# Optimization experiments

Hardware: AMD Instinct MI355X
Metric: run time of the kernel (lower is better)

Reference implementation:

```python
import jax, jax.numpy as jnp
from jax import lax
import numpy as np

VOCAB, TAGS, EMB, HID = 50000, 45, 256, 512
B, S = 32, 256


def setup_inputs() -> dict:
    key = jax.random.key(0)
    ks = jax.random.split(key, 12)
    sc = 0.05
    return {
        "x": jax.random.randint(ks[0], (B, S), 0, VOCAB),
        "tags": jax.random.randint(ks[1], (B, S), 0, TAGS),
        "emb": jax.random.normal(ks[2], (VOCAB, EMB), jnp.float32) * sc,
        "w_ih_f": jax.random.normal(ks[3], (4 * HID, EMB), jnp.float32) * sc,
        "w_hh_f": jax.random.normal(ks[4], (4 * HID, HID), jnp.float32) * sc,
        "b_f": jnp.zeros((4 * HID,), jnp.float32),
        "w_ih_b": jax.random.normal(ks[5], (4 * HID, EMB), jnp.float32) * sc,
        "w_hh_b": jax.random.normal(ks[6], (4 * HID, HID), jnp.float32) * sc,
        "b_b": jnp.zeros((4 * HID,), jnp.float32),
        "lin_w": jax.random.normal(ks[7], (TAGS, 2 * HID), jnp.float32) * sc,
        "lin_b": jnp.zeros((TAGS,), jnp.float32),
        "start_t": jax.random.normal(ks[8], (TAGS,), jnp.float32) * 0.1,
        "end_t": jax.random.normal(ks[9], (TAGS,), jnp.float32) * 0.1,
        "trans": jax.random.normal(ks[10], (TAGS,), jnp.float32)[:, None] * 0.0 + jax.random.normal(ks[11], (TAGS, TAGS), jnp.float32) * 0.1,
    }


def _lstm_dir(xs, w_ih, w_hh, b, reverse):
    # xs: [B,S,E]. PyTorch gate order: i, f, g, o.
    Bsz = xs.shape[0]
    H = w_hh.shape[1]
    def step(carry, x_t):
        h, c = carry
        g = x_t @ w_ih.T + h @ w_hh.T + b
        i, f, gg, o = jnp.split(g, 4, axis=-1)
        c = jax.nn.sigmoid(f) * c + jax.nn.sigmoid(i) * jnp.tanh(gg)
        h = jax.nn.sigmoid(o) * jnp.tanh(c)
        return (h, c), h
    init = (jnp.zeros((Bsz, H), xs.dtype), jnp.zeros((Bsz, H), xs.dtype))
    _, hs = lax.scan(step, init, jnp.swapaxes(xs, 0, 1), reverse=reverse)
    return jnp.swapaxes(hs, 0, 1)  # [B,S,H]


def _crf_nll(em, tags, start_t, end_t, trans):
    # em: [B,S,T]; numerator: score of gold path
    em_sc = jnp.take_along_axis(em, tags[..., None], axis=2)[..., 0].sum(axis=1)
    tr_sc = trans[tags[:, :-1], tags[:, 1:]].sum(axis=1)
    score = start_t[tags[:, 0]] + em_sc + tr_sc + end_t[tags[:, -1]]
    # partition function via forward algorithm (logsumexp recurrence)
    alpha0 = start_t + em[:, 0]  # [B,T]
    def step(alpha, e_t):
        alpha = jax.nn.logsumexp(alpha[:, :, None] + trans[None], axis=1) + e_t
        return alpha, None
    alpha, _ = lax.scan(step, alpha0, jnp.swapaxes(em[:, 1:], 0, 1))
    logZ = jax.nn.logsumexp(alpha + end_t, axis=1)
    return -(score - logZ).mean()  # reduction='mean', loss = -llh


def reference(x, tags, emb, w_ih_f, w_hh_f, b_f, w_ih_b, w_hh_b, b_b,
              lin_w, lin_b, start_t, end_t, trans):
    embeds = emb[x]                               # [B,S,E]
    h_f = _lstm_dir(embeds, w_ih_f, w_hh_f, b_f, False)
    h_b = _lstm_dir(embeds, w_ih_b, w_hh_b, b_b, True)
    lstm_out = jnp.concatenate([h_f, h_b], axis=-1)  # [B,S,2H]
    emissions = lstm_out @ lin_w.T + lin_b           # [B,S,T]
    return _crf_nll(emissions, tags, start_t, end_t, trans)
```

## Files before the change

kernel.cpp:

```cpp
#include <hip/hip_runtime.h>

#define BB 32
#define SS 256
#define EMBD 256
#define HIDD 512
#define NTAG 45
#define TPAD 48
#define NBLK 32
#define APAD 520
#define GRID_REC 256

typedef __bf16 bf16x8 __attribute__((ext_vector_type(8)));
typedef float  f32x4  __attribute__((ext_vector_type(4)));
typedef short  s16x8  __attribute__((ext_vector_type(8)));
typedef short  s16x4  __attribute__((ext_vector_type(4)));

__device__ __forceinline__ unsigned short f2bf(float x) {
  unsigned u = __builtin_bit_cast(unsigned, x);
  u = (u + 0x7fffu + ((u >> 16) & 1u)) >> 16;
  return (unsigned short)u;
}
__device__ __forceinline__ float bf2f(unsigned short u) {
  unsigned v = ((unsigned)u) << 16; return __builtin_bit_cast(float, v);
}
__device__ __forceinline__ float ftanh(float x) {
  float e = __expf(2.f * x);
  return 1.f - 2.f / (e + 1.f);
}

__device__ __forceinline__ unsigned ld32_cpol(const unsigned* p, bool sys) {
  unsigned v;
  if (sys) asm volatile("global_load_dword %0, %1, off sc0 sc1\ns_waitcnt vmcnt(0)"
                        : "=v"(v) : "v"(p) : "memory");
  else     asm volatile("global_load_dword %0, %1, off sc0\ns_waitcnt vmcnt(0)"
                        : "=v"(v) : "v"(p) : "memory");
  return v;
}
__device__ __forceinline__ void st32_cpol(unsigned* p, unsigned v, bool sys) {
  if (sys) asm volatile("global_store_dword %0, %1, off sc0 sc1" :: "v"(p), "v"(v) : "memory");
  else     asm volatile("global_store_dword %0, %1, off sc0"     :: "v"(p), "v"(v) : "memory");
}

#define LD8(CPOL)                                                           \
  asm volatile("global_load_dwordx4 %0, %[q0], off " CPOL "\n\t"            \
               "global_load_dwordx4 %1, %[q1], off " CPOL "\n\t"            \
               "global_load_dwordx4 %2, %[q2], off " CPOL "\n\t"            \
               "global_load_dwordx4 %3, %[q3], off " CPOL "\n\t"            \
               "global_load_dwordx4 %4, %[q4], off " CPOL "\n\t"            \
               "global_load_dwordx4 %5, %[q5], off " CPOL "\n\t"            \
               "global_load_dwordx4 %6, %[q6], off " CPOL "\n\t"            \
               "global_load_dwordx4 %7, %[q7], off " CPOL "\n\t"            \
               "s_waitcnt vmcnt(0)"                                         \
               : "=&v"(v0), "=&v"(v1), "=&v"(v2), "=&v"(v3),                \
                 "=&v"(v4), "=&v"(v5), "=&v"(v6), "=&v"(v7)                 \
               : [q0] "v"(p), [q1] "v"(p + 2048), [q2] "v"(p + 4096),       \
                 [q3] "v"(p + 6144), [q4] "v"(p + 8192), [q5] "v"(p + 10240),\
                 [q6] "v"(p + 12288), [q7] "v"(p + 14336)                   \
               : "memory")

__global__ void k_pack_e(const int* __restrict__ x, const float* __restrict__ emb,
                         unsigned short* __restrict__ E) {
  int idx = blockIdx.x * 256 + threadIdx.x;
  int e = idx & 255; int bt = idx >> 8; int b = bt & 31; int t = bt >> 5;
  int tok = x[b * SS + t];
  E[idx] = f2bf(emb[(long)tok * EMBD + e]);
}

__global__ void k_pack_w(const float* __restrict__ wih_f, const float* __restrict__ whh_f,
                         const float* __restrict__ bf_,  const float* __restrict__ wih_b,
                         const float* __restrict__ whh_b, const float* __restrict__ bb_,
                         unsigned short* __restrict__ Wh, unsigned short* __restrict__ Wie,
                         float* __restrict__ Bh) {
  long idx = (long)blockIdx.x * 256 + threadIdx.x;
  int k = (int)(idx % 768); long rest = idx / 768;
  int r2 = (int)(rest & 2047); int dir = (int)(rest >> 11);
  int blk = r2 >> 6, rl = r2 & 63, gate = rl >> 4, hl = rl & 15;
  int orig = gate * HIDD + blk * 16 + hl;
  const float* wih = dir ? wih_b : wih_f;
  const float* whh = dir ? whh_b : whh_f;
  if (k < HIDD) Wh[((long)(dir * 2048 + r2)) * 512 + k] = f2bf(whh[(long)orig * HIDD + k]);
  else          Wie[((long)(dir * 2048 + r2)) * 256 + (k - 512)] = f2bf(wih[(long)orig * EMBD + (k - 512)]);
  if (k == 0) {
    const float* bias = dir ? bb_ : bf_;
    Bh[dir * 2048 + r2] = bias[orig];
  }
}

__global__ void k_pack_l(const float* __restrict__ lin_w, const float* __restrict__ lin_b,
                         unsigned short* __restrict__ LW, float* __restrict__ LB) {
  int idx = blockIdx.x * 256 + threadIdx.x;
  if (idx < TPAD * 1024) {
    int tag = idx >> 10; int c = idx & 1023;
    LW[idx] = (tag < NTAG) ? f2bf(lin_w[tag * 1024 + c]) : (unsigned short)0;
  } else if (idx < TPAD * 1024 + TPAD) {
    int tag = idx - TPAD * 1024;
    LB[tag] = (tag < NTAG) ? lin_b[tag] : 0.f;
  }
}

__launch_bounds__(256)
__global__ void k_eproj(const unsigned short* __restrict__ E,
                        const unsigned short* __restrict__ Wie,
                        const float* __restrict__ Bh,
                        unsigned short* __restrict__ Ep) {
  __shared__ unsigned short W2[64 * 264];
  const int bx = blockIdx.x;
  const int tg = bx & 63, blk = (bx >> 6) & 31, dir = bx >> 11;
  const int tid = threadIdx.x;
  const int w = tid >> 6, lane = tid & 63;
  const int lm = lane & 15, quad = lane >> 4;

  {
    const unsigned short* src = Wie + ((long)(dir * 2048 + blk * 64)) * 256;
    for (int i = 0; i < 8; ++i) {
      int c = i * 256 + tid;
      int row = c >> 5, off = c & 31;
      *(s16x8*)&W2[row * 264 + off * 8] = *(const s16x8*)&src[row * 256 + off * 8];
    }
  }
  __syncthreads();

  f32x4 acc[2][4] = {};
#pragma unroll
  for (int kk = 0; kk < 8; ++kk) {
    s16x8 av[2];
#pragma unroll
    for (int sub = 0; sub < 2; ++sub)
      av[sub] = *(const s16x8*)&E[((long)(tg * 128 + w * 32 + sub * 16 + lm)) * 256 + kk * 32 + quad * 8];
#pragma unroll
    for (int sub = 0; sub < 2; ++sub)
#pragma unroll
      for (int n = 0; n < 4; ++n) {
        s16x8 bs = *(const s16x8*)&W2[(n * 16 + lm) * 264 + kk * 32 + quad * 8];
        acc[sub][n] = __builtin_amdgcn_mfma_f32_16x16x32_bf16(
            __builtin_bit_cast(bf16x8, av[sub]), __builtin_bit_cast(bf16x8, bs), acc[sub][n], 0, 0, 0);
      }
  }
  float bh[4];
#pragma unroll
  for (int n = 0; n < 4; ++n) bh[n] = Bh[dir * 2048 + blk * 64 + n * 16 + lm];

  const int t = tg * 4 + w;
#pragma unroll
  for (int sub = 0; sub < 2; ++sub)
#pragma unroll
    for (int n = 0; n < 4; ++n) {
      s16x4 pk;
#pragma unroll
      for (int r = 0; r < 4; ++r) pk[r] = (short)f2bf(acc[sub][n][r] + bh[n]);
      int tidc = (sub * 2 + (n >> 1)) * 64 + quad * 16 + lm;
      *(s16x4*)&Ep[(((long)(dir * 32 + blk) * SS + t) * 256 + tidc) * 8 + (n & 1) * 4] = pk;
    }
}

__launch_bounds__(256, 1)
__global__ void k_rec(const unsigned short* __restrict__ Wh,
                      const unsigned short* __restrict__ Ep,
                      unsigned short* __restrict__ H,
                      unsigned int* __restrict__ sync) {
  __shared__ unsigned short A_ls[32 * APAD];
  __shared__ float G_ls[32 * 66 + 4608];
  __shared__ int fast_ls;

  const int bx = blockIdx.x;
  const int role = bx & 7;
  if (role >= 2) return;
  const int dir = role;
  const int blk = bx >> 3;
  const int tid = threadIdx.x;
  const int w = tid >> 6, lane = tid & 63;
  const int lm = lane & 15, quad = lane >> 4;
  const int mt = w >> 1, nt = w & 1;

  unsigned int* det   = sync;
  unsigned int* flags = sync + 64;

  s16x8 wb[2][16];
  {
    const unsigned short* wsrc =
        Wh + ((long)(dir * 2048 + blk * 64 + nt * 32 + lm)) * 512 + quad * 8;
#pragma unroll
    for (int ns = 0; ns < 2; ++ns)
#pragma unroll
      for (int kk = 0; kk < 16; ++kk)
        wb[ns][kk] = *(const s16x8*)&wsrc[ns * 16 * 512 + kk * 32];
  }

  unsigned xcc;
  asm volatile("s_getreg_b32 %0, hwreg(HW_REG_XCC_ID)" : "=s"(xcc));
  if (tid == 0) st32_cpol(&det[dir * 32 + blk], xcc | 0x100u, true);
  if (w == 0) {
    unsigned v;
    for (;;) {
      v = (lane < 32) ? ld32_cpol(&det[dir * 32 + lane], true) : (xcc | 0x100u);
      if (__ballot(v != 0u) == ~0ull) break;
      __builtin_amdgcn_s_sleep(1);
    }
    if (lane == 0) fast_ls = (__ballot(v == (xcc | 0x100u)) == ~0ull) ? 1 : 0;
  }
  __syncthreads();
  const bool fast = (fast_ls != 0);
  __threadfence();

  const int gb = tid >> 3, hp = tid & 7;
  float c0 = 0.f, c1 = 0.f;

  unsigned short* Hd = H + (long)dir * SS * BB * HIDD;
  unsigned int* flagd = flags + dir * SS * NBLK;
  const unsigned short* Epd = Ep + (long)(dir * 32 + blk) * SS * 2048;

  for (int t = 0; t < SS; ++t) {
    const int tE = (dir == 0) ? t : (SS - 1 - t);

    s16x8 ecur = *(const s16x8*)&Epd[((long)tE * 256 + tid) * 8];

    f32x4 acc0 = {0.f, 0.f, 0.f, 0.f}, acc1 = {0.f, 0.f, 0.f, 0.f};
    if (t > 0) {
      if (w == 0) {
        const unsigned int* fl = flagd + (long)(t - 1) * NBLK;
        for (;;) {
          unsigned f = (lane < 32) ? ld32_cpol(&fl[lane], !fast) : 1u;
          if (__ballot(f != 0u) == ~0ull) break;
          __builtin_amdgcn_s_sleep(1);
        }
      }
      __syncthreads();
      {
        const int hslot = (dir == 0) ? (t - 1) : (SS - t);
        const unsigned short* p = Hd + (long)hslot * BB * HIDD + w * 512 + lane * 8;
        s16x8 v0, v1, v2, v3, v4, v5, v6, v7;
        if (fast) { LD8("sc0"); } else { LD8("sc0 sc1"); }
        unsigned short* d = &A_ls[w * APAD + lane * 8];
        *(s16x8*)(d + 0 * 2080) = v0; *(s16x8*)(d + 1 * 2080) = v1;
        *(s16x8*)(d + 2 * 2080) = v2; *(s16x8*)(d + 3 * 2080) = v3;
        *(s16x8*)(d + 4 * 2080) = v4; *(s16x8*)(d + 5 * 2080) = v5;
        *(s16x8*)(d + 6 * 2080) = v6; *(s16x8*)(d + 7 * 2080) = v7;
      }
      __syncthreads();
#pragma unroll
      for (int kk = 0; kk < 16; ++kk) {
        s16x8 av = *(const s16x8*)&A_ls[(mt * 16 + lm) * APAD + kk * 32 + quad * 8];
        acc0 = __builtin_amdgcn_mfma_f32_16x16x32_bf16(
            __builtin_bit_cast(bf16x8, av), __builtin_bit_cast(bf16x8, wb[0][kk]), acc0, 0, 0, 0);
        acc1 = __builtin_amdgcn_mfma_f32_16x16x32_bf16(
            __builtin_bit_cast(bf16x8, av), __builtin_bit_cast(bf16x8, wb[1][kk]), acc1, 0, 0, 0);
      }
    }
#pragma unroll
    for (int r = 0; r < 4; ++r) {
      int mm = mt * 16 + quad * 4 + r;
      G_ls[mm * 66 + nt * 32 + lm]      = acc0[r] + bf2f((unsigned short)ecur[r]);
      G_ls[mm * 66 + nt * 32 + 16 + lm] = acc1[r] + bf2f((unsigned short)ecur[4 + r]);
    }
    __syncthreads();
    {
      float gi0 = G_ls[gb * 66 + 0  + 2 * hp], gi1 = G_ls[gb * 66 + 0  + 2 * hp + 1];
      float gf0 = G_ls[gb * 66 + 16 + 2 * hp], gf1 = G_ls[gb * 66 + 16 + 2 * hp + 1];
      float gg0 = G_ls[gb * 66 + 32 + 2 * hp], gg1 = G_ls[gb * 66 + 32 + 2 * hp + 1];
      float go0 = G_ls[gb * 66 + 48 + 2 * hp], go1 = G_ls[gb * 66 + 48 + 2 * hp + 1];
      float si0 = 1.f / (1.f + __expf(-gi0)), si1 = 1.f / (1.f + __expf(-gi1));
      float sf0 = 1.f / (1.f + __expf(-gf0)), sf1 = 1.f / (1.f + __expf(-gf1));
      float so0 = 1.f / (1.f + __expf(-go0)), so1 = 1.f / (1.f + __expf(-go1));
      float tg0 = ftanh(gg0), tg1 = ftanh(gg1);
      c0 = sf0 * c0 + si0 * tg0;
      c1 = sf1 * c1 + si1 * tg1;
      float h0 = so0 * ftanh(c0), h1 = so1 * ftanh(c1);
      int tslot = (dir == 0) ? t : (SS - 1 - t);
      unsigned hv = (unsigned)f2bf(h0) | ((unsigned)f2bf(h1) << 16);
      st32_cpol((unsigned*)&Hd[(long)tslot * BB * HIDD + (long)gb * HIDD + blk * 16 + 2 * hp],
                hv, !fast);
    }
    __syncthreads();
    if (t < SS - 1 && tid == 0)
      st32_cpol(&flagd[(long)t * NBLK + blk], 1u, !fast);
  }
}

__launch_bounds__(256)
__global__ void k_emis(const unsigned short* __restrict__ H,
                       const unsigned short* __restrict__ LW,
                       const float* __restrict__ LB,
                       float* __restrict__ EM) {
  const int row0 = blockIdx.x * 32;
  const int tid = threadIdx.x;
  const int w = tid >> 6, lane = tid & 63;
  const int lm = lane & 15, quad = lane >> 4;
  const unsigned short* Hf = H;
  const unsigned short* Hb = H + (long)SS * BB * HIDD;

  for (int tile = w; tile < 6; tile += 4) {
    int mt = tile / 3, nt = tile % 3;
    int arow = row0 + mt * 16 + lm;
    int nrow = nt * 16 + lm;
    f32x4 acc = {0.f, 0.f, 0.f, 0.f};
#pragma unroll 4
    for (int kk = 0; kk < 32; ++kk) {
      int k0 = kk * 32 + quad * 8;
      s16x8 asv = (k0 < HIDD) ? *(const s16x8*)&Hf[(long)arow * HIDD + k0]
                              : *(const s16x8*)&Hb[(long)arow * HIDD + (k0 - HIDD)];
      s16x8 bsv = *(const s16x8*)&LW[nrow * 1024 + k0];
      acc = __builtin_amdgcn_mfma_f32_16x16x32_bf16(
          __builtin_bit_cast(bf16x8, asv), __builtin_bit_cast(bf16x8, bsv), acc, 0, 0, 0);
    }
    float bias = LB[nrow];
#pragma unroll
    for (int r = 0; r < 4; ++r) {
      int mm = row0 + mt * 16 + quad * 4 + r;
      EM[(long)mm * TPAD + nrow] = acc[r] + bias;
    }
  }
}

__global__ void k_crf(const int* __restrict__ tags, const float* __restrict__ start_t,
                      const float* __restrict__ end_t, const float* __restrict__ trans,
                      const float* __restrict__ EM, float* __restrict__ chain) {
  __shared__ float T_ls[NTAG * TPAD];
  __shared__ float ET[48 * 48 + 16];
  __shared__ float P_ls[64];
  const int b = blockIdx.x;
  const int lane = threadIdx.x;
  const int j = lane;

  for (int i = lane; i < NTAG * NTAG; i += 64)
    T_ls[(i / NTAG) * TPAD + (i % NTAG)] = trans[i];
  for (int i = lane; i < 48 * 48 + 16; i += 64) ET[i] = 0.f;
  __syncthreads();

  float Mj = -1e30f;
  if (j < NTAG) {
    for (int i = 0; i < NTAG; ++i) Mj = fmaxf(Mj, T_ls[i * TPAD + j]);
    for (int i = 0; i < NTAG; ++i) ET[i * 48 + j] = __expf(T_ls[i * TPAD + j] - Mj);
  }
  __syncthreads();

  float et[48];
#pragma unroll
  for (int i = 0; i < 48; ++i) et[i] = ET[i * 48 + j];

  float part = 0.f;
  for (int t = lane; t < SS; t += 64) {
    int tg = tags[b * SS + t];
    part += EM[((long)t * BB + b) * TPAD + tg];
    if (t + 1 < SS) part += T_ls[tg * TPAD + tags[b * SS + t + 1]];
    if (t == 0)      part += start_t[tg];
    if (t == SS - 1) part += end_t[tg];
  }
  for (int off = 32; off; off >>= 1) part += __shfl_down(part, off);
  float score = __shfl(part, 0);

  float alpha = (j < NTAG) ? (start_t[j] + EM[(long)b * TPAD + j]) : -1e30f;
  float e_next = (j < NTAG) ? EM[((long)BB + b) * TPAD + j] : 0.f;
  for (int t = 1; t < SS; ++t) {
    float e_cur = e_next;
    if (t < SS - 1) e_next = (j < NTAG) ? EM[((long)(t + 1) * BB + b) * TPAD + j] : 0.f;
    float am = alpha;
#pragma unroll
    for (int off = 32; off; off >>= 1) am = fmaxf(am, __shfl_xor(am, off));
    float p = __expf(alpha - am);
    P_ls[lane] = p;
    __builtin_amdgcn_wave_barrier();
    float s0 = 0.f, s1 = 0.f, s2 = 0.f, s3 = 0.f;
#pragma unroll
    for (int i0 = 0; i0 < 48; i0 += 4) {
      f32x4 pv = *(const f32x4*)&P_ls[i0];
      s0 += pv.x * et[i0];
      s1 += pv.y * et[i0 + 1];
      s2 += pv.z * et[i0 + 2];
      s3 += pv.w * et[i0 + 3];
    }
    __builtin_amdgcn_wave_barrier();
    float s = (s0 + s1) + (s2 + s3);
    float na = am + Mj + __logf(s) + e_cur;
    alpha = (j < NTAG) ? na : -1e30f;
  }
  float v = (j < NTAG) ? (alpha + end_t[j]) : -1e30f;
  float mx = v;
  for (int off = 32; off; off >>= 1) mx = fmaxf(mx, __shfl_xor(mx, off));
  float s = __expf(v - mx);
  for (int off = 32; off; off >>= 1) s += __shfl_xor(s, off);
  if (lane == 0) chain[b] = score - (mx + __logf(s));
}

__global__ void k_fin(const float* __restrict__ chain, float* __restrict__ out) {
  int lane = threadIdx.x;
  float v = (lane < BB) ? chain[lane] : 0.f;
  for (int off = 32; off; off >>= 1) v += __shfl_xor(v, off);
  if (lane == 0) out[0] = -v / (float)BB;
}

extern "C" void kernel_launch(void* const* d_in, const int* in_sizes, int n_in,
                              void* d_out, int out_size, void* d_ws, size_t ws_size,
                              hipStream_t stream) {
  const int*   x      = (const int*)d_in[0];
  const int*   tags   = (const int*)d_in[1];
  const float* emb    = (const float*)d_in[2];
  const float* wih_f  = (const float*)d_in[3];
  const float* whh_f  = (const float*)d_in[4];
  const float* b_f    = (const float*)d_in[5];
  const float* wih_b  = (const float*)d_in[6];
  const float* whh_b  = (const float*)d_in[7];
  const float* b_b    = (const float*)d_in[8];
  const float* lin_w  = (const float*)d_in[9];
  const float* lin_b  = (const float*)d_in[10];
  const float* start_t= (const float*)d_in[11];
  const float* end_t  = (const float*)d_in[12];
  const float* trans  = (const float*)d_in[13];

  char* ws = (char*)d_ws;
  size_t off = 0;
  auto alloc = [&](size_t bytes) {
    void* p = ws + off; off = (off + bytes + 255) & ~(size_t)255; return p;
  };
  size_t sync_bytes = (64 + 2 * SS * NBLK) * 4;
  unsigned int*   sync = (unsigned int*) alloc(sync_bytes);
  unsigned short* E   = (unsigned short*)alloc((size_t)SS * BB * EMBD * 2);
  unsigned short* Wh  = (unsigned short*)alloc((size_t)2 * 2048 * 512 * 2);
  unsigned short* Wie = (unsigned short*)alloc((size_t)2 * 2048 * 256 * 2);
  float*          Bh  = (float*)         alloc((size_t)2 * 2048 * 4);
  unsigned short* Ep  = (unsigned short*)alloc((size_t)2 * 32 * SS * 2048 * 2);
  unsigned short* H   = (unsigned short*)alloc((size_t)2 * SS * BB * HIDD * 2);
  unsigned short* LW  = (unsigned short*)alloc((size_t)TPAD * 1024 * 2);
  float*          LB  = (float*)         alloc((size_t)TPAD * 4);
  float*          EM  = (float*)         alloc((size_t)SS * BB * TPAD * 4);
  float*          chain = (float*)       alloc((size_t)BB * 4);

  hipMemsetAsync(sync, 0, sync_bytes, stream);
  k_pack_e<<<dim3((SS * BB * EMBD) / 256), dim3(256), 0, stream>>>(x, emb, E);
  k_pack_w<<<dim3((2 * 2048 * 768) / 256), dim3(256), 0, stream>>>(
      wih_f, whh_f, b_f, wih_b, whh_b, b_b, Wh, Wie, Bh);
  k_pack_l<<<dim3((TPAD * 1024 + TPAD + 255) / 256), dim3(256), 0, stream>>>(
      lin_w, lin_b, LW, LB);
  k_eproj<<<dim3(4096), dim3(256), 0, stream>>>(E, Wie, Bh, Ep);

  void* kargs[] = {&Wh, &Ep, &H, &sync};
  hipLaunchCooperativeKernel((const void*)k_rec, dim3(GRID_REC), dim3(256), kargs, 0, stream);

  k_emis<<<dim3((SS * BB) / 32), dim3(256), 0, stream>>>(H, LW, LB, EM);
  k_crf<<<dim3(BB), dim3(64), 0, stream>>>(tags, start_t, end_t, trans, EM, chain);
  k_fin<<<dim3(1), dim3(64), 0, stream>>>(chain, (float*)d_out);
}
```

Measured before the change: 1.067 ms.

## Replace per-step flag barrier with sequence-tagged ring buffer for hidden state exchange

Each block now publishes its hidden-state pairs together with a step counter into a four-deep ring buffer (reusing the embedding scratch space). Consumers poll the data itself, checking the tags, instead of waiting on separate completion flags and then reloading H. This removes the flag store, a block-wide barrier, and a dependent load round-trip from the serial recurrence chain. In exchange every thread polls twice as many bytes, and correctness depends on the dwordx2 store being seen atomically and on ring slots not being overwritten before slower readers consume them.

```diff
diff --git a/kernel.cpp b/kernel.cpp
--- a/kernel.cpp
+++ b/kernel.cpp
@@ -9,11 +9,14 @@
 #define NBLK 32
 #define APAD 520
 #define GRID_REC 256
+#define RDEPTH 4
 
 typedef __bf16 bf16x8 __attribute__((ext_vector_type(8)));
 typedef float  f32x4  __attribute__((ext_vector_type(4)));
 typedef short  s16x8  __attribute__((ext_vector_type(8)));
 typedef short  s16x4  __attribute__((ext_vector_type(4)));
+typedef unsigned u32x4 __attribute__((ext_vector_type(4)));
+typedef unsigned u32x2 __attribute__((ext_vector_type(2)));
 
 __device__ __forceinline__ unsigned short f2bf(float x) {
   unsigned u = __builtin_bit_cast(unsigned, x);
@@ -41,22 +44,32 @@
   else     asm volatile("global_store_dword %0, %1, off sc0"     :: "v"(p), "v"(v) : "memory");
 }
 
-#define LD8(CPOL)                                                           \
-  asm volatile("global_load_dwordx4 %0, %[q0], off " CPOL "\n\t"            \
-               "global_load_dwordx4 %1, %[q1], off " CPOL "\n\t"            \
-               "global_load_dwordx4 %2, %[q2], off " CPOL "\n\t"            \
-               "global_load_dwordx4 %3, %[q3], off " CPOL "\n\t"            \
-               "global_load_dwordx4 %4, %[q4], off " CPOL "\n\t"            \
-               "global_load_dwordx4 %5, %[q5], off " CPOL "\n\t"            \
-               "global_load_dwordx4 %6, %[q6], off " CPOL "\n\t"            \
-               "global_load_dwordx4 %7, %[q7], off " CPOL "\n\t"            \
-               "s_waitcnt vmcnt(0)"                                         \
-               : "=&v"(v0), "=&v"(v1), "=&v"(v2), "=&v"(v3),                \
-                 "=&v"(v4), "=&v"(v5), "=&v"(v6), "=&v"(v7)                 \
-               : [q0] "v"(p), [q1] "v"(p + 2048), [q2] "v"(p + 4096),       \
-                 [q3] "v"(p + 6144), [q4] "v"(p + 8192), [q5] "v"(p + 10240),\
-                 [q6] "v"(p + 12288), [q7] "v"(p + 14336)                   \
-               : "memory")
+#define POLL16(CPOL)                                                        \
+  asm volatile(                                                             \
+    "global_load_dwordx4 %0, %[b0], off offset:-2048 " CPOL "\n\t"          \
+    "global_load_dwordx4 %1, %[b0], off offset:2048 " CPOL "\n\t"           \
+    "global_load_dwordx4 %2, %[b1], off offset:-2048 " CPOL "\n\t"          \
+    "global_load_dwordx4 %3, %[b1], off offset:2048 " CPOL "\n\t"           \
+    "global_load_dwordx4 %4, %[b2], off offset:-2048 " CPOL "\n\t"          \
+    "global_load_dwordx4 %5, %[b2], off offset:2048 " CPOL "\n\t"           \
+    "global_load_dwordx4 %6, %[b3], off offset:-2048 " CPOL "\n\t"          \
+    "global_load_dwordx4 %7, %[b3], off offset:2048 " CPOL "\n\t"           \
+    "global_load_dwordx4 %8, %[b4], off offset:-2048 " CPOL "\n\t"          \
+    "global_load_dwordx4 %9, %[b4], off offset:2048 " CPOL "\n\t"           \
+    "global_load_dwordx4 %10, %[b5], off offset:-2048 " CPOL "\n\t"         \
+    "global_load_dwordx4 %11, %[b5], off offset:2048 " CPOL "\n\t"          \
+    "global_load_dwordx4 %12, %[b6], off offset:-2048 " CPOL "\n\t"         \
+    "global_load_dwordx4 %13, %[b6], off offset:2048 " CPOL "\n\t"          \
+    "global_load_dwordx4 %14, %[b7], off offset:-2048 " CPOL "\n\t"         \
+    "global_load_dwordx4 %15, %[b7], off offset:2048 " CPOL "\n\t"          \
+    "s_waitcnt vmcnt(0)"                                                    \
+    : "=&v"(p0), "=&v"(p1), "=&v"(p2), "=&v"(p3),                           \
+      "=&v"(p4), "=&v"(p5), "=&v"(p6), "=&v"(p7),                           \
+      "=&v"(p8), "=&v"(p9), "=&v"(p10), "=&v"(p11),                         \
+      "=&v"(p12), "=&v"(p13), "=&v"(p14), "=&v"(p15)                        \
+    : [b0] "v"(bq0), [b1] "v"(bq1), [b2] "v"(bq2), [b3] "v"(bq3),           \
+      [b4] "v"(bq4), [b5] "v"(bq5), [b6] "v"(bq6), [b7] "v"(bq7)            \
+    : "memory")
 
 __global__ void k_pack_e(const int* __restrict__ x, const float* __restrict__ emb,
                          unsigned short* __restrict__ E) {
@@ -157,6 +170,7 @@
 __global__ void k_rec(const unsigned short* __restrict__ Wh,
                       const unsigned short* __restrict__ Ep,
                       unsigned short* __restrict__ H,
+                      unsigned long long* __restrict__ RING,
                       unsigned int* __restrict__ sync) {
   __shared__ unsigned short A_ls[32 * APAD];
   __shared__ float G_ls[32 * 66 + 4608];
@@ -172,8 +186,7 @@
   const int lm = lane & 15, quad = lane >> 4;
   const int mt = w >> 1, nt = w & 1;
 
-  unsigned int* det   = sync;
-  unsigned int* flags = sync + 64;
+  unsigned int* det = sync;
 
   s16x8 wb[2][16];
   {
@@ -206,8 +219,11 @@
   float c0 = 0.f, c1 = 0.f;
 
   unsigned short* Hd = H + (long)dir * SS * BB * HIDD;
-  unsigned int* flagd = flags + dir * SS * NBLK;
+  unsigned long long* Rd = RING + (long)dir * RDEPTH * BB * 256;
   const unsigned short* Epd = Ep + (long)(dir * 32 + blk) * SS * 2048;
+
+  const int rsel = lane >> 5;
+  const int psel = (lane & 31) << 1;
 
   for (int t = 0; t < SS; ++t) {
     const int tE = (dir == 0) ? t : (SS - 1 - t);
@@ -216,25 +232,59 @@
 
     f32x4 acc0 = {0.f, 0.f, 0.f, 0.f}, acc1 = {0.f, 0.f, 0.f, 0.f};
     if (t > 0) {
-      if (w == 0) {
-        const unsigned int* fl = flagd + (long)(t - 1) * NBLK;
+      {
+        const int slot = (t - 1) & (RDEPTH - 1);
+        const unsigned* bp =
+            (const unsigned*)(Rd + ((long)slot * BB + rsel) * 256 + w * 64 + psel);
+        const unsigned* bq0 = bp + 512;
+        const unsigned* bq1 = bp + 1 * 2048 + 512;
+        const unsigned* bq2 = bp + 2 * 2048 + 512;
+        const unsigned* bq3 = bp + 3 * 2048 + 512;
+        const unsigned* bq4 = bp + 4 * 2048 + 512;
+        const unsigned* bq5 = bp + 5 * 2048 + 512;
+        const unsigned* bq6 = bp + 6 * 2048 + 512;
+        const unsigned* bq7 = bp + 7 * 2048 + 512;
+        const unsigned exp_ = (unsigned)t;
+        u32x4 p0, p1, p2, p3, p4, p5, p6, p7, p8, p9, p10, p11, p12, p13, p14, p15;
         for (;;) {
-          unsigned f = (lane < 32) ? ld32_cpol(&fl[lane], !fast) : 1u;
-          if (__ballot(f != 0u) == ~0ull) break;
+          if (fast) { POLL16("sc0"); } else { POLL16("sc0 sc1"); }
+          unsigned ok = 1u;
+          ok &= (unsigned)(p0.y == exp_)  & (unsigned)(p0.w == exp_);
+          ok &= (unsigned)(p1.y == exp_)  & (unsigned)(p1.w == exp_);
+          ok &= (unsigned)(p2.y == exp_)  & (unsigned)(p2.w == exp_);
+          ok &= (unsigned)(p3.y == exp_)  & (unsigned)(p3.w == exp_);
+          ok &= (unsigned)(p4.y == exp_)  & (unsigned)(p4.w == exp_);
+          ok &= (unsigned)(p5.y == exp_)  & (unsigned)(p5.w == exp_);
+          ok &= (unsigned)(p6.y == exp_)  & (unsigned)(p6.w == exp_);
+          ok &= (unsigned)(p7.y == exp_)  & (unsigned)(p7.w == exp_);
+          ok &= (unsigned)(p8.y == exp_)  & (unsigned)(p8.w == exp_);
+          ok &= (unsigned)(p9.y == exp_)  & (unsigned)(p9.w == exp_);
+          ok &= (unsigned)(p10.y == exp_) & (unsigned)(p10.w == exp_);
+          ok &= (unsigned)(p11.y == exp_) & (unsigned)(p11.w == exp_);
+          ok &= (unsigned)(p12.y == exp_) & (unsigned)(p12.w == exp_);
+          ok &= (unsigned)(p13.y == exp_) & (unsigned)(p13.w == exp_);
+          ok &= (unsigned)(p14.y == exp_) & (unsigned)(p14.w == exp_);
+          ok &= (unsigned)(p15.y == exp_) & (unsigned)(p15.w == exp_);
+          if (__ballot(ok != 0u) == ~0ull) break;
           __builtin_amdgcn_s_sleep(1);
         }
-      }
-      __syncthreads();
-      {
-        const int hslot = (dir == 0) ? (t - 1) : (SS - t);
-        const unsigned short* p = Hd + (long)hslot * BB * HIDD + w * 512 + lane * 8;
-        s16x8 v0, v1, v2, v3, v4, v5, v6, v7;
-        if (fast) { LD8("sc0"); } else { LD8("sc0 sc1"); }
-        unsigned short* d = &A_ls[w * APAD + lane * 8];
-        *(s16x8*)(d + 0 * 2080) = v0; *(s16x8*)(d + 1 * 2080) = v1;
-        *(s16x8*)(d + 2 * 2080) = v2; *(s16x8*)(d + 3 * 2080) = v3;
-        *(s16x8*)(d + 4 * 2080) = v4; *(s16x8*)(d + 5 * 2080) = v5;
-        *(s16x8*)(d + 6 * 2080) = v6; *(s16x8*)(d + 7 * 2080) = v7;
+        unsigned short* dbase = &A_ls[rsel * APAD + w * 128 + (lane & 31) * 4];
+        *(u32x2*)(dbase + 0  * 2 * APAD) = (u32x2){p0.x,  p0.z};
+        *(u32x2*)(dbase + 1  * 2 * APAD) = (u32x2){p1.x,  p1.z};
+        *(u32x2*)(dbase + 2  * 2 * APAD) = (u32x2){p2.x,  p2.z};
+        *(u32x2*)(dbase + 3  * 2 * APAD) = (u32x2){p3.x,  p3.z};
+        *(u32x2*)(dbase + 4  * 2 * APAD) = (u32x2){p4.x,  p4.z};
+        *(u32x2*)(dbase + 5  * 2 * APAD) = (u32x2){p5.x,  p5.z};
+        *(u32x2*)(dbase + 6  * 2 * APAD) = (u32x2){p6.x,  p6.z};
+        *(u32x2*)(dbase + 7  * 2 * APAD) = (u32x2){p7.x,  p7.z};
+        *(u32x2*)(dbase + 8  * 2 * APAD) = (u32x2){p8.x,  p8.z};
+        *(u32x2*)(dbase + 9  * 2 * APAD) = (u32x2){p9.x,  p9.z};
+        *(u32x2*)(dbase + 10 * 2 * APAD) = (u32x2){p10.x, p10.z};
+        *(u32x2*)(dbase + 11 * 2 * APAD) = (u32x2){p11.x, p11.z};
+        *(u32x2*)(dbase + 12 * 2 * APAD) = (u32x2){p12.x, p12.z};
+        *(u32x2*)(dbase + 13 * 2 * APAD) = (u32x2){p13.x, p13.z};
+        *(u32x2*)(dbase + 14 * 2 * APAD) = (u32x2){p14.x, p14.z};
+        *(u32x2*)(dbase + 15 * 2 * APAD) = (u32x2){p15.x, p15.z};
       }
       __syncthreads();
 #pragma unroll
@@ -267,12 +317,12 @@
       float h0 = so0 * ftanh(c0), h1 = so1 * ftanh(c1);
       int tslot = (dir == 0) ? t : (SS - 1 - t);
       unsigned hv = (unsigned)f2bf(h0) | ((unsigned)f2bf(h1) << 16);
-      st32_cpol((unsigned*)&Hd[(long)tslot * BB * HIDD + (long)gb * HIDD + blk * 16 + 2 * hp],
-                hv, !fast);
-    }
-    __syncthreads();
-    if (t < SS - 1 && tid == 0)
-      st32_cpol(&flagd[(long)t * NBLK + blk], 1u, !fast);
+      *(unsigned*)&Hd[(long)tslot * BB * HIDD + (long)gb * HIDD + blk * 16 + 2 * hp] = hv;
+      u32x2 pv; pv.x = hv; pv.y = (unsigned)(t + 1);
+      unsigned long long* dst = Rd + ((long)(t & (RDEPTH - 1)) * BB + gb) * 256 + blk * 8 + hp;
+      if (fast) asm volatile("global_store_dwordx2 %0, %1, off sc0"     :: "v"(dst), "v"(pv) : "memory");
+      else      asm volatile("global_store_dwordx2 %0, %1, off sc0 sc1" :: "v"(dst), "v"(pv) : "memory");
+    }
   }
 }
 
@@ -411,7 +461,7 @@
   auto alloc = [&](size_t bytes) {
     void* p = ws + off; off = (off + bytes + 255) & ~(size_t)255; return p;
   };
-  size_t sync_bytes = (64 + 2 * SS * NBLK) * 4;
+  size_t sync_bytes = 64 * 4;
   unsigned int*   sync = (unsigned int*) alloc(sync_bytes);
   unsigned short* E   = (unsigned short*)alloc((size_t)SS * BB * EMBD * 2);
   unsigned short* Wh  = (unsigned short*)alloc((size_t)2 * 2048 * 512 * 2);
@@ -424,6 +474,9 @@
   float*          EM  = (float*)         alloc((size_t)SS * BB * TPAD * 4);
   float*          chain = (float*)       alloc((size_t)BB * 4);
 
+  unsigned long long* RING = (unsigned long long*)E;
+  size_t ring_bytes = (size_t)2 * RDEPTH * BB * 256 * 8;
+
   hipMemsetAsync(sync, 0, sync_bytes, stream);
   k_pack_e<<<dim3((SS * BB * EMBD) / 256), dim3(256), 0, stream>>>(x, emb, E);
   k_pack_w<<<dim3((2 * 2048 * 768) / 256), dim3(256), 0, stream>>>(
@@ -431,8 +484,9 @@
   k_pack_l<<<dim3((TPAD * 1024 + TPAD + 255) / 256), dim3(256), 0, stream>>>(
       lin_w, lin_b, LW, LB);
   k_eproj<<<dim3(4096), dim3(256), 0, stream>>>(E, Wie, Bh, Ep);
-
-  void* kargs[] = {&Wh, &Ep, &H, &sync};
+  hipMemsetAsync(RING, 0, ring_bytes, stream);
+
+  void* kargs[] = {&Wh, &Ep, &H, &RING, &sync};
   hipLaunchCooperativeKernel((const void*)k_rec, dim3(GRID_REC), dim3(256), kargs, 0, stream);
 
   k_emis<<<dim3((SS * BB) / 32), dim3(256), 0, stream>>>(H, LW, LB, EM);
```

New measurement: 1.381 ms. +29.4%, slower.
